# Optimization experiments

Measured on AMD Instinct MI355X. Metric: run time of the kernel, lower is better.

Reference implementation:

```python
import jax, jax.numpy as jnp
import numpy as np

H = 4  # head_num
K_CONV = 1  # convolution_num


def mhsa_mean(x, Wq, Wk, Wv, Wo):
    # x: [..., L, d]; standard multi-head self-attention followed by mean over L
    d = x.shape[-1]
    hd = d // H
    q = (x @ Wq).reshape(x.shape[:-1] + (H, hd))
    k = (x @ Wk).reshape(x.shape[:-1] + (H, hd))
    v = (x @ Wv).reshape(x.shape[:-1] + (H, hd))
    scores = jnp.einsum('...lhd,...mhd->...hlm', q, k) / jnp.sqrt(jnp.asarray(hd, x.dtype))
    attn = jax.nn.softmax(scores, axis=-1)
    o = jnp.einsum('...hlm,...mhd->...lhd', attn, v).reshape(x.shape) @ Wo
    return o.mean(axis=-2)


def setup_inputs() -> dict:
    key = jax.random.key(0)
    ks = jax.random.split(key, 18)
    WORD, QUERY, ENT, REV = 50000, 50000, 100000, 100000
    DW, DE = 64, 64
    LQ, LR, E, B = 8, 8, 2000000, 1024
    W_word = jax.random.normal(ks[0], (WORD, DW), jnp.float32) * 0.02
    W_word = W_word.at[0].set(0.0)  # padding_idx=0
    W_query = jax.random.normal(ks[1], (QUERY, DE), jnp.float32) * 0.02
    W_entity = jax.random.normal(ks[2], (ENT, DE), jnp.float32) * 0.02
    Wq = jax.random.normal(ks[3], (DW, DW), jnp.float32) * 0.05
    Wk = jax.random.normal(ks[4], (DW, DW), jnp.float32) * 0.05
    Wv = jax.random.normal(ks[5], (DW, DW), jnp.float32) * 0.05
    Wo = jax.random.normal(ks[6], (DW, DW), jnp.float32) * 0.05
    query_word_ids = jax.random.randint(ks[7], (QUERY, LQ), 0, WORD)
    review_word_ids = jax.random.randint(ks[8], (REV, LR), 0, WORD)
    profile_dst = jax.random.randint(ks[9], (REV,), 0, ENT)
    p_src = jax.random.randint(ks[10], (E,), 0, ENT)
    p_dst = jax.random.randint(ks[11], (E,), 0, ENT)
    p_qid = jax.random.randint(ks[12], (E,), 0, QUERY)
    users = jax.random.randint(ks[13], (B,), 0, ENT)
    items = jax.random.randint(ks[14], (B,), 0, ENT)
    negs = jax.random.randint(ks[15], (B,), 0, ENT)
    query_words = jax.random.randint(ks[16], (B, LQ), 0, WORD)
    return {'W_word': W_word, 'W_query': W_query, 'W_entity': W_entity,
            'Wq': Wq, 'Wk': Wk, 'Wv': Wv, 'Wo': Wo,
            'query_word_ids': query_word_ids, 'review_word_ids': review_word_ids,
            'profile_dst': profile_dst, 'p_src': p_src, 'p_dst': p_dst, 'p_qid': p_qid,
            'users': users, 'items': items, 'negs': negs, 'query_words': query_words}


def reference(W_word, W_query, W_entity, Wq, Wk, Wv, Wo,
              query_word_ids, review_word_ids, profile_dst, p_src, p_dst, p_qid,
              users, items, negs, query_words):
    N = W_entity.shape[0]
    DE = W_query.shape[1]
    # --- doc embeddings via MHSA+mean over composing words ---
    h_query = mhsa_mean(W_word[query_word_ids], Wq, Wk, Wv, Wo)    # [Q, DW]
    h_review = mhsa_mean(W_word[review_word_ids], Wq, Wk, Wv, Wo)  # [R, DW]
    # --- profiles: sum reviews into entities, degree-normalize ---
    deg_p = jnp.maximum(jax.ops.segment_sum(jnp.ones(profile_dst.shape[0], jnp.float32), profile_dst, num_segments=N), 1.0)
    ent_h = jax.ops.segment_sum(h_review, profile_dst, num_segments=N) / deg_p[:, None]
    q_e0 = jnp.concatenate([W_query, h_query], axis=-1)   # [Q, D]
    e_k = jnp.concatenate([W_entity, ent_h], axis=-1)     # e_0 [N, D]
    # --- interaction degrees: out-deg(purchased) + out-deg(purchased_by) ---
    ones_e = jnp.ones(p_src.shape[0], jnp.float32)
    deg_i = jax.ops.segment_sum(ones_e, p_src, num_segments=N) + jax.ops.segment_sum(ones_e, p_dst, num_segments=N)
    inv_sqrt = 1.0 / jnp.sqrt(jnp.maximum(deg_i, 1.0))    # [N]
    q_edge = q_e0[p_qid]                                   # [E, D]
    e_acc = e_k
    for _ in range(K_CONV):
        # purchased: m = src.e_k + q_e0[q_id] / sqrt(deg_i[src]); sum to dst
        msg = e_k[p_src] + q_edge * inv_sqrt[p_src][:, None]
        agg = jax.ops.segment_sum(msg, p_dst, num_segments=N)
        # purchased_by (reverse edges): m = e_k[src]/sqrt(deg_i[src]); sum to dst
        agg = agg + jax.ops.segment_sum(e_k[p_dst] * inv_sqrt[p_dst][:, None], p_src, num_segments=N)
        e_k = agg * inv_sqrt[:, None]
        e_acc = e_acc + e_k
    e = e_acc / (K_CONV + 1)                               # [N, D]
    # --- batch forward (train mode) ---
    qb = mhsa_mean(W_word[query_words], Wq, Wk, Wv, Wo)    # [B, DW]
    qb = jnp.concatenate([jnp.zeros((qb.shape[0], DE), qb.dtype), qb], axis=-1)
    personalized = e[users] + qb
    return personalized, e[items], e[negs]
```

## Files before the change

kernel.cpp:

```cpp
#include <hip/hip_runtime.h>

typedef unsigned int uint;
typedef unsigned short ushort;

typedef __bf16 bf16x8 __attribute__((ext_vector_type(8)));
typedef float f32x4 __attribute__((ext_vector_type(4)));
union U8 { uint4 u4; uint w[4]; bf16x8 b; };

__device__ __forceinline__ float bf2f(ushort u) {
    return __uint_as_float(((uint)u) << 16);
}
__device__ __forceinline__ float2 bfp2f(uint u) {
    float2 r;
    r.x = __uint_as_float(u << 16);
    r.y = __uint_as_float(u & 0xffff0000u);
    return r;
}
__device__ __forceinline__ ushort f2bf(float f) {
    uint u = __float_as_uint(f);
    return (ushort)((u + 0x7fffu + ((u >> 16) & 1u)) >> 16);
}
__device__ __forceinline__ uint4 pack8(float4 a, float4 b) {
    uint4 u;
    u.x = (uint)f2bf(a.x) | ((uint)f2bf(a.y) << 16);
    u.y = (uint)f2bf(a.z) | ((uint)f2bf(a.w) << 16);
    u.z = (uint)f2bf(b.x) | ((uint)f2bf(b.y) << 16);
    u.w = (uint)f2bf(b.z) | ((uint)f2bf(b.w) << 16);
    return u;
}

__global__ void setup_kernel(const float* __restrict__ Wq,
                             const float* __restrict__ Wk,
                             const float* __restrict__ Wv,
                             const float* __restrict__ Wo,
                             ushort* __restrict__ wsw, ushort* __restrict__ wswo,
                             const int* __restrict__ users,
                             const int* __restrict__ items,
                             const int* __restrict__ negs,
                             int* __restrict__ mapid, int* __restrict__ mcnt,
                             int B) {
    int bid = blockIdx.x;
    if (bid < 64) {
        int e = bid * 256 + threadIdx.x;
        if (e < 12288) {
            int f = e >> 9, r = e & 511;
            int lane = r >> 3, i = r & 7;
            int ct = f >> 1, kh = f & 1;
            int k = kh * 32 + (lane >> 4) * 8 + i;
            int col = (ct & 3) * 16 + (lane & 15);
            const float* W = ct < 4 ? Wq : (ct < 8 ? Wk : Wv);
            wsw[f * 512 + lane * 8 + i] = f2bf(W[k * 64 + col]);
        } else if (e < 16384) {
            int e2 = e - 12288;
            int f = e2 >> 9, r = e2 & 511;
            int lane = r >> 3, i = r & 7;
            int ct = f >> 1, kh = f & 1;
            int k = kh * 32 + (lane >> 4) * 8 + i;
            int col = ct * 16 + (lane & 15);
            wswo[f * 512 + lane * 8 + i] = f2bf(Wo[k * 64 + col]);
        }
        return;
    }
    int t = (bid - 64) * 256 + threadIdx.x;
    if (t >= 3 * B) return;
    int n = t < B ? users[t] : (t < 2 * B ? items[t - B] : negs[t - 2 * B]);
    int old = atomicCAS(&mapid[n], -1, -2);
    if (old == -1) mapid[n] = atomicAdd(mcnt, 1);
}

__global__ void pre_kernel(const float* __restrict__ W_word,
                           const ushort* __restrict__ wsw,
                           ushort* __restrict__ Pq, ushort* __restrict__ Pk,
                           ushort* __restrict__ Pv,
                           const float* __restrict__ W_query,
                           const float* __restrict__ W_entity,
                           ushort* __restrict__ qe0b, ushort* __restrict__ e0b,
                           const int* __restrict__ p_src,
                           const int* __restrict__ p_dst,
                           const int* __restrict__ profile_dst,
                           const int* __restrict__ mapid,
                           int* __restrict__ degp, int* __restrict__ deg2,
                           int WORD, int Qn, int N, int E, int R,
                           int nc_blk, int npj_blk, int ncq_blk, int nce_blk) {
    int bid = blockIdx.x;
    int g = bid >> 3, j = bid & 7;
    if ((g & 3) == 3) {
        int idx = (g >> 2) * 8 + j;
        if (idx >= nc_blk) return;
        int base = idx * 1024 + threadIdx.x;
#pragma unroll
        for (int k = 0; k < 4; k++) {
            int t = base + k * 256;
            if (t < E) {
                int s = p_src[t], d = p_dst[t];
                int md = mapid[d]; if (md >= 0) atomicAdd(&deg2[md], 1);
                int ms = mapid[s]; if (ms >= 0) atomicAdd(&deg2[ms], 1);
            }
            if (t < R) atomicAdd(&degp[profile_dst[t]], 1);
        }
        return;
    }
    int idx = ((g >> 2) * 3 + (g & 3)) * 8 + j;
    if (idx < npj_blk) {
        int tile = idx * 4 + (threadIdx.x >> 6);
        if (tile * 16 >= WORD) return;
        int lane = threadIdx.x & 63, l15 = lane & 15, gi = lane >> 4;
        const float* xr = W_word + ((size_t)tile * 16 + l15) * 64 + gi * 8;
        U8 a0, a1;
        a0.u4 = pack8(*(const float4*)(xr), *(const float4*)(xr + 4));
        a1.u4 = pack8(*(const float4*)(xr + 32), *(const float4*)(xr + 36));
        const f32x4 zero4 = {0.f, 0.f, 0.f, 0.f};
#pragma unroll
        for (int ct = 0; ct < 12; ct++) {
            U8 b0, b1;
            b0.u4 = *(const uint4*)(wsw + (ct * 2 + 0) * 512 + lane * 8);
            b1.u4 = *(const uint4*)(wsw + (ct * 2 + 1) * 512 + lane * 8);
            f32x4 acc = __builtin_amdgcn_mfma_f32_16x16x32_bf16(a0.b, b0.b, zero4, 0, 0, 0);
            acc = __builtin_amdgcn_mfma_f32_16x16x32_bf16(a1.b, b1.b, acc, 0, 0, 0);
            ushort* dst = ct < 4 ? Pq : (ct < 8 ? Pk : Pv);
            int col = (ct & 3) * 16 + l15;
#pragma unroll
            for (int r = 0; r < 4; r++)
                dst[((size_t)tile * 16 + gi * 4 + r) * 64 + col] = f2bf(acc[r]);
        }
    } else if (idx < npj_blk + ncq_blk) {
        int t = (idx - npj_blk) * 256 + threadIdx.x;
        if (t >= Qn * 16) return;
        int r = t >> 4, c = (t & 15) * 4;
        const float4 v = *(const float4*)(W_query + (size_t)r * 64 + c);
        ushort4 o;
        o.x = f2bf(v.x); o.y = f2bf(v.y); o.z = f2bf(v.z); o.w = f2bf(v.w);
        *(ushort4*)(qe0b + (size_t)r * 128 + c) = o;
    } else if (idx < npj_blk + ncq_blk + nce_blk) {
        int t = (idx - npj_blk - ncq_blk) * 256 + threadIdx.x;
        if (t >= N * 16) return;
        int r = t >> 4, c = (t & 15) * 4;
        const float4 v = *(const float4*)(W_entity + (size_t)r * 64 + c);
        ushort4 o;
        o.x = f2bf(v.x); o.y = f2bf(v.y); o.z = f2bf(v.z); o.w = f2bf(v.w);
        *(ushort4*)(e0b + (size_t)r * 128 + c) = o;
    }
}

__global__ void scan_sum(const int* __restrict__ degp, int* __restrict__ csum,
                         int N) {
    __shared__ int red[4];
    int chunk = blockIdx.x, t = threadIdx.x;
    int base = chunk * 1024;
    int v = 0;
#pragma unroll
    for (int k = 0; k < 4; k++) {
        int idx = base + t * 4 + k;
        if (idx < N) v += degp[idx];
    }
#pragma unroll
    for (int o = 32; o; o >>= 1) v += __shfl_down(v, o, 64);
    if ((t & 63) == 0) red[t >> 6] = v;
    __syncthreads();
    if (t == 0) csum[chunk] = red[0] + red[1] + red[2] + red[3];
}

__global__ void scan_mid(int* __restrict__ csum, int nchunk,
                         const int* __restrict__ deg2,
                         int* __restrict__ offs2, int* __restrict__ cursor2,
                         int nb2) {
    __shared__ int lds[256];
    int t = threadIdx.x;
    int v = (t < nchunk) ? csum[t] : 0;
    lds[t] = v;
    __syncthreads();
    for (int o = 1; o < 256; o <<= 1) {
        int u = (t >= o) ? lds[t - o] : 0;
        __syncthreads();
        lds[t] += u;
        __syncthreads();
    }
    if (t < nchunk) csum[t] = lds[t] - v;
    __syncthreads();
    int k2 = nb2 >> 8;
    int s = 0;
    for (int k = 0; k < k2; k++) s += deg2[t * k2 + k];
    lds[t] = s;
    __syncthreads();
    for (int o = 1; o < 256; o <<= 1) {
        int u = (t >= o) ? lds[t - o] : 0;
        __syncthreads();
        lds[t] += u;
        __syncthreads();
    }
    int tb = lds[t] - s;
    for (int k = 0; k < k2; k++) {
        int dv = deg2[t * k2 + k];
        offs2[t * k2 + k] = tb;
        cursor2[t * k2 + k] = tb;
        tb += dv;
    }
    if (t == 255) offs2[nb2] = tb;
}

__global__ void scan_chunk(const int* __restrict__ degp,
                           const int* __restrict__ csum,
                           int* __restrict__ offs_r, int* __restrict__ cursor_r,
                           int N) {
    __shared__ int lds[256];
    int chunk = blockIdx.x, t = threadIdx.x;
    int base = chunk * 1024 + t * 4;
    int v0 = (base + 0 < N) ? degp[base + 0] : 0;
    int v1 = (base + 1 < N) ? degp[base + 1] : 0;
    int v2 = (base + 2 < N) ? degp[base + 2] : 0;
    int v3 = (base + 3 < N) ? degp[base + 3] : 0;
    int s = v0 + v1 + v2 + v3;
    lds[t] = s;
    __syncthreads();
    for (int o = 1; o < 256; o <<= 1) {
        int u = (t >= o) ? lds[t - o] : 0;
        __syncthreads();
        lds[t] += u;
        __syncthreads();
    }
    int tb = lds[t] - s + csum[chunk];
    int vv[4] = {v0, v1, v2, v3};
#pragma unroll
    for (int k = 0; k < 4; k++) {
        int idx = base + k;
        if (idx < N) {
            offs_r[idx] = tb; cursor_r[idx] = tb; tb += vv[k];
            if (idx == N - 1) offs_r[N] = tb;
        }
    }
}

__device__ __forceinline__ void mhsa_pair(const ushort* __restrict__ Pq,
                                          const ushort* __restrict__ Pk,
                                          const ushort* __restrict__ Pv,
                                          const int* __restrict__ ids,
                                          int wid2, int lane,
                                          ushort* __restrict__ outb) {
    const int l15 = lane & 15;
    const int gi  = lane >> 4;
    const int hs  = gi >> 1;
    const int dbase = (gi & 1) * 8;
    const int* idr = ids + (size_t)wid2 * 16;
    const bool valid = hs == (l15 >> 3);

    const int myid = idr[l15];
    int vid[8];
#pragma unroll
    for (int i = 0; i < 8; i++) vid[i] = idr[dbase + i];

    uint pk4[4][2];
    const f32x4 zero4 = {0.f, 0.f, 0.f, 0.f};
#pragma unroll
    for (int h = 0; h < 4; h++) {
        U8 a, b;
        if (valid) {
            a.u4 = *(const uint4*)(Pk + (size_t)myid * 64 + h * 16 + dbase);
            b.u4 = *(const uint4*)(Pq + (size_t)myid * 64 + h * 16 + dbase);
        } else {
            a.u4 = make_uint4(0, 0, 0, 0);
            b.u4 = make_uint4(0, 0, 0, 0);
        }
        f32x4 d = __builtin_amdgcn_mfma_f32_16x16x32_bf16(a.b, b.b, zero4, 0, 0, 0);
        float s0 = d[0] * 0.25f, s1 = d[1] * 0.25f;
        float s2 = d[2] * 0.25f, s3 = d[3] * 0.25f;
        if (!valid) { s0 = s1 = s2 = s3 = -1e30f; }
        float mx = fmaxf(fmaxf(s0, s1), fmaxf(s2, s3));
        mx = fmaxf(mx, __shfl_xor(mx, 16, 64));
        mx = fmaxf(mx, __shfl_xor(mx, 32, 64));
        float x0 = __expf(s0 - mx), x1 = __expf(s1 - mx);
        float x2 = __expf(s2 - mx), x3 = __expf(s3 - mx);
        float sm = x0 + x1 + x2 + x3;
        sm += __shfl_xor(sm, 16, 64);
        sm += __shfl_xor(sm, 32, 64);
        float f = 0.125f / sm;
        uint w0 = (uint)f2bf(x0 * f) | ((uint)f2bf(x1 * f) << 16);
        uint w1 = (uint)f2bf(x2 * f) | ((uint)f2bf(x3 * f) << 16);
        pk4[h][0] = valid ? w0 : 0u;
        pk4[h][1] = valid ? w1 : 0u;
    }

    const int srcA = l15 + (gi & 1) * 32;
    const int srcB = srcA + 16;
    const bool hi = gi >= 2;
    size_t vb[8];
#pragma unroll
    for (int i = 0; i < 8; i++) vb[i] = (size_t)vid[i] * 64;
#pragma unroll
    for (int t = 0; t < 4; t++) {
        uint aw0 = (uint)__shfl((int)pk4[t][0], srcA, 64);
        uint aw1 = (uint)__shfl((int)pk4[t][1], srcA, 64);
        uint aw2 = (uint)__shfl((int)pk4[t][0], srcB, 64);
        uint aw3 = (uint)__shfl((int)pk4[t][1], srcB, 64);
        U8 av_;
        av_.w[0] = hi ? 0u : aw0; av_.w[1] = hi ? 0u : aw1;
        av_.w[2] = hi ? 0u : aw2; av_.w[3] = hi ? 0u : aw3;
        uint e[8];
#pragma unroll
        for (int i = 0; i < 8; i++)
            e[i] = hi ? 0u : (uint)Pv[vb[i] + t * 16 + l15];
        U8 bv;
        bv.w[0] = e[0] | (e[1] << 16);
        bv.w[1] = e[2] | (e[3] << 16);
        bv.w[2] = e[4] | (e[5] << 16);
        bv.w[3] = e[6] | (e[7] << 16);
        f32x4 acc = __builtin_amdgcn_mfma_f32_16x16x32_bf16(av_.b, bv.b, zero4, 0, 0, 0);
        float s = acc[0] + acc[1] + acc[2] + acc[3];
        s += __shfl_xor(s, 16, 64);
        if ((gi & 1) == 0) {
            int row = wid2 * 2 + hs;
            outb[(size_t)row * 64 + t * 16 + l15] = f2bf(s);
        }
    }
}

__global__ void mega_kernel(const ushort* __restrict__ Pq,
                            const ushort* __restrict__ Pk,
                            const ushort* __restrict__ Pv,
                            const int* __restrict__ query_word_ids,
                            const int* __restrict__ review_word_ids,
                            const int* __restrict__ query_words,
                            ushort* __restrict__ hqom,
                            ushort* __restrict__ hrev,
                            ushort* __restrict__ omb,
                            const int* __restrict__ p_src,
                            const int* __restrict__ p_dst,
                            const int* __restrict__ p_qid,
                            const int* __restrict__ profile_dst,
                            const int* __restrict__ mapid,
                            int* __restrict__ degc8,
                            int* __restrict__ cursor2, int2* __restrict__ list2,
                            int* __restrict__ cursor_r, int* __restrict__ rmsg,
                            int Qn, int R, int B, int E, int N,
                            int nr_blk, int nq_blk, int nb_blk,
                            int nd_blk, int np_blk, int nv_blk) {
    int bid = blockIdx.x;
    int g = bid >> 3, j = bid & 7;
    int idx = (g >> 1) * 8 + j;
    if (g & 1) {
        if (idx < nd_blk) {
            int* degc = degc8 + (size_t)(bid & 7) * N;
            int base = idx * 1024 + threadIdx.x;
#pragma unroll
            for (int k = 0; k < 4; k++) {
                int t = base + k * 256;
                if (t < E) {
                    atomicAdd(&degc[p_src[t]], 1);
                    atomicAdd(&degc[p_dst[t]], 1);
                }
            }
        } else if (idx < nd_blk + np_blk) {
            int base = (idx - nd_blk) * 512 + threadIdx.x;
#pragma unroll
            for (int k = 0; k < 2; k++) {
                int e = base + k * 256;
                if (e < E) {
                    int s = p_src[e], d = p_dst[e];
                    int md = mapid[d], ms = mapid[s];
                    if (md >= 0)
                        list2[atomicAdd(&cursor2[md], 1)] = make_int2(s, p_qid[e]);
                    if (ms >= 0)
                        list2[atomicAdd(&cursor2[ms], 1)] = make_int2(d, -1);
                }
            }
        } else if (idx < nd_blk + np_blk + nv_blk) {
            int r = (idx - nd_blk - np_blk) * 256 + threadIdx.x;
            if (r >= R) return;
            rmsg[atomicAdd(&cursor_r[profile_dst[r]], 1)] = r;
        }
        return;
    }
    int lane = threadIdx.x & 63;
    int w = threadIdx.x >> 6;
    if (idx < nr_blk) {
        int wid2 = idx * 4 + w;
        if (wid2 < (R >> 1))
            mhsa_pair(Pq, Pk, Pv, review_word_ids, wid2, lane, hrev);
    } else if (idx < nr_blk + nq_blk) {
        int wid2 = (idx - nr_blk) * 4 + w;
        if (wid2 < (Qn >> 1))
            mhsa_pair(Pq, Pk, Pv, query_word_ids, wid2, lane, hqom);
    } else if (idx < nr_blk + nq_blk + nb_blk) {
        int wid2 = (idx - nr_blk - nq_blk) * 4 + w;
        if (wid2 < (B >> 1))
            mhsa_pair(Pq, Pk, Pv, query_words, wid2, lane, omb);
    }
}

__device__ __forceinline__ void wo_tile(int tile,
                                        const ushort* __restrict__ eom,
                                        const ushort* __restrict__ hqom,
                                        const ushort* __restrict__ omb,
                                        const ushort* __restrict__ wswo,
                                        ushort* __restrict__ e0b,
                                        ushort* __restrict__ qe0b,
                                        float* __restrict__ qb,
                                        int N, int Qn, int lane) {
    int l15 = lane & 15, gi = lane >> 4;
    int row0 = tile << 4;
    int region; int rb;
    const ushort* src;
    if (row0 < N)            { region = 0; rb = row0;            src = eom; }
    else if (row0 < N + Qn)  { region = 1; rb = row0 - N;        src = hqom; }
    else                     { region = 2; rb = row0 - N - Qn;   src = omb; }
    const ushort* sr = src + ((size_t)rb + l15) * 64;
    U8 a0, a1;
    a0.u4 = *(const uint4*)(sr + gi * 8);
    a1.u4 = *(const uint4*)(sr + 32 + gi * 8);
    const f32x4 zero4 = {0.f, 0.f, 0.f, 0.f};
#pragma unroll
    for (int ct = 0; ct < 4; ct++) {
        U8 b0, b1;
        b0.u4 = *(const uint4*)(wswo + (ct * 2 + 0) * 512 + lane * 8);
        b1.u4 = *(const uint4*)(wswo + (ct * 2 + 1) * 512 + lane * 8);
        f32x4 acc = __builtin_amdgcn_mfma_f32_16x16x32_bf16(a0.b, b0.b, zero4, 0, 0, 0);
        acc = __builtin_amdgcn_mfma_f32_16x16x32_bf16(a1.b, b1.b, acc, 0, 0, 0);
        int col = ct * 16 + l15;
#pragma unroll
        for (int r = 0; r < 4; r++) {
            int row = rb + gi * 4 + r;
            if (region == 0)      e0b[(size_t)row * 128 + 64 + col] = f2bf(acc[r]);
            else if (region == 1) qe0b[(size_t)row * 128 + 64 + col] = f2bf(acc[r]);
            else                  qb[(size_t)row * 64 + col] = acc[r];
        }
    }
}

__global__ void post1_kernel(const ushort* __restrict__ hrev,
                             const int* __restrict__ offs_r,
                             const int* __restrict__ rmsg,
                             ushort* __restrict__ eom,
                             const ushort* __restrict__ hqom,
                             const ushort* __restrict__ omb,
                             const ushort* __restrict__ wswo,
                             ushort* __restrict__ e0b, ushort* __restrict__ qe0b,
                             float* __restrict__ qb,
                             const int* __restrict__ degc8,
                             float* __restrict__ inv,
                             int N, int Qn, int B,
                             int nent_blk, int nwo_blk) {
    int bid = blockIdx.x;
    if (bid < nent_blk) {
        int g = (bid * 256 + (int)threadIdx.x) >> 4;
        int c = (threadIdx.x & 15) * 4;
        if (g >= N) return;
        int beg = offs_r[g], end = offs_r[g + 1];
        float a0 = 0.f, a1 = 0.f, a2 = 0.f, a3 = 0.f;
        for (int m = beg; m < end; m++) {
            int r = rmsg[m];
            ushort4 v = *(const ushort4*)(hrev + (size_t)r * 64 + c);
            a0 += bf2f(v.x); a1 += bf2f(v.y); a2 += bf2f(v.z); a3 += bf2f(v.w);
        }
        float s = 1.0f / (float)max(end - beg, 1);
        ushort4 o;
        o.x = f2bf(a0 * s); o.y = f2bf(a1 * s); o.z = f2bf(a2 * s); o.w = f2bf(a3 * s);
        *(ushort4*)(eom + (size_t)g * 64 + c) = o;
    } else if (bid < nent_blk + nwo_blk) {
        int ntile = (N + Qn + B) >> 4;
        int tile = (N >> 4) + (bid - nent_blk) * 4 + ((int)threadIdx.x >> 6);
        if (tile >= ntile) return;
        wo_tile(tile, eom, hqom, omb, wswo, e0b, qe0b, qb, N, Qn,
                threadIdx.x & 63);
    } else {
        int t = (bid - nent_blk - nwo_blk) * 256 + threadIdx.x;
        if (t >= N) return;
        int s = 0;
#pragma unroll
        for (int c = 0; c < 8; c++) s += degc8[(size_t)c * N + t];
        inv[t] = 1.0f / sqrtf((float)max(s, 1));
    }
}

__global__ void post2_kernel(const ushort* __restrict__ eom,
                             const ushort* __restrict__ hqom,
                             const ushort* __restrict__ omb,
                             const ushort* __restrict__ wswo,
                             ushort* __restrict__ e0b, ushort* __restrict__ qe0b,
                             float* __restrict__ qb, int N, int Qn, int B) {
    int tile = blockIdx.x * 4 + ((int)threadIdx.x >> 6);
    if (tile >= (N >> 4)) return;
    wo_tile(tile, eom, hqom, omb, wswo, e0b, qe0b, qb, N, Qn, threadIdx.x & 63);
}

__global__ void gather_out(const ushort* __restrict__ e0b,
                           const ushort* __restrict__ qe0b,
                           const float* __restrict__ inv,
                           const int* __restrict__ mapid,
                           const int* __restrict__ offs2,
                           const int2* __restrict__ list2,
                           const float* __restrict__ qb,
                           const int* __restrict__ users,
                           const int* __restrict__ items,
                           const int* __restrict__ negs,
                           float* __restrict__ out, int B) {
    int slot = (blockIdx.x * blockDim.x + threadIdx.x) >> 4;
    int c = (threadIdx.x & 15) * 8;
    if (slot >= 3 * B) return;
    int which = slot / B, b = slot - which * B;
    int node = which == 0 ? users[b] : (which == 1 ? items[b] : negs[b]);
    int m = mapid[node];
    int beg = offs2[m], end = offs2[m + 1];
    float a0 = 0.f, a1 = 0.f, a2 = 0.f, a3 = 0.f;
    float a4 = 0.f, a5 = 0.f, a6 = 0.f, a7 = 0.f;
    for (int i = beg; i < end; i++) {
        int2 mm = list2[i];
        float w = inv[mm.x];
        const uint4 ev = *(const uint4*)(e0b + (size_t)mm.x * 128 + c);
        if (mm.y >= 0) {
            const uint4 qv = *(const uint4*)(qe0b + (size_t)mm.y * 128 + c);
            float2 e, q;
            e = bfp2f(ev.x); q = bfp2f(qv.x); a0 += fmaf(q.x, w, e.x); a1 += fmaf(q.y, w, e.y);
            e = bfp2f(ev.y); q = bfp2f(qv.y); a2 += fmaf(q.x, w, e.x); a3 += fmaf(q.y, w, e.y);
            e = bfp2f(ev.z); q = bfp2f(qv.z); a4 += fmaf(q.x, w, e.x); a5 += fmaf(q.y, w, e.y);
            e = bfp2f(ev.w); q = bfp2f(qv.w); a6 += fmaf(q.x, w, e.x); a7 += fmaf(q.y, w, e.y);
        } else {
            float2 e;
            e = bfp2f(ev.x); a0 = fmaf(e.x, w, a0); a1 = fmaf(e.y, w, a1);
            e = bfp2f(ev.y); a2 = fmaf(e.x, w, a2); a3 = fmaf(e.y, w, a3);
            e = bfp2f(ev.z); a4 = fmaf(e.x, w, a4); a5 = fmaf(e.y, w, a5);
            e = bfp2f(ev.w); a6 = fmaf(e.x, w, a6); a7 = fmaf(e.y, w, a7);
        }
    }
    float wn = inv[node];
    const uint4 sv = *(const uint4*)(e0b + (size_t)node * 128 + c);
    float2 e0v;
    float r0, r1, r2, r3, r4, r5, r6, r7;
    e0v = bfp2f(sv.x); r0 = 0.5f * fmaf(a0, wn, e0v.x); r1 = 0.5f * fmaf(a1, wn, e0v.y);
    e0v = bfp2f(sv.y); r2 = 0.5f * fmaf(a2, wn, e0v.x); r3 = 0.5f * fmaf(a3, wn, e0v.y);
    e0v = bfp2f(sv.z); r4 = 0.5f * fmaf(a4, wn, e0v.x); r5 = 0.5f * fmaf(a5, wn, e0v.y);
    e0v = bfp2f(sv.w); r6 = 0.5f * fmaf(a6, wn, e0v.x); r7 = 0.5f * fmaf(a7, wn, e0v.y);
    if (which == 0 && c >= 64) {
        const float4 q0 = *(const float4*)(qb + (size_t)b * 64 + (c - 64));
        const float4 q1 = *(const float4*)(qb + (size_t)b * 64 + (c - 60));
        r0 += q0.x; r1 += q0.y; r2 += q0.z; r3 += q0.w;
        r4 += q1.x; r5 += q1.y; r6 += q1.z; r7 += q1.w;
    }
    float* dst = out + (size_t)which * B * 128 + (size_t)b * 128 + c;
    float4 w0; w0.x = r0; w0.y = r1; w0.z = r2; w0.w = r3;
    float4 w1; w1.x = r4; w1.y = r5; w1.z = r6; w1.w = r7;
    *(float4*)dst = w0;
    *(float4*)(dst + 4) = w1;
}

extern "C" void kernel_launch(void* const* d_in, const int* in_sizes, int n_in,
                              void* d_out, int out_size, void* d_ws, size_t ws_size,
                              hipStream_t stream) {
    const float* W_word   = (const float*)d_in[0];
    const float* W_query  = (const float*)d_in[1];
    const float* W_entity = (const float*)d_in[2];
    const float* Wq       = (const float*)d_in[3];
    const float* Wk       = (const float*)d_in[4];
    const float* Wv       = (const float*)d_in[5];
    const float* Wo       = (const float*)d_in[6];
    const int* query_word_ids  = (const int*)d_in[7];
    const int* review_word_ids = (const int*)d_in[8];
    const int* profile_dst     = (const int*)d_in[9];
    const int* p_src  = (const int*)d_in[10];
    const int* p_dst  = (const int*)d_in[11];
    const int* p_qid  = (const int*)d_in[12];
    const int* users  = (const int*)d_in[13];
    const int* items  = (const int*)d_in[14];
    const int* negs   = (const int*)d_in[15];
    const int* query_words = (const int*)d_in[16];

    const int WORD = in_sizes[0] / 64;
    const int Qn   = in_sizes[1] / 64;
    const int N    = in_sizes[2] / 64;
    const int R    = in_sizes[8] / 8;
    const int E    = in_sizes[10];
    const int B    = in_sizes[13];

    const int NB2 = ((3 * B + 255) / 256) * 256;

    ushort* e0b  = (ushort*)d_ws;
    ushort* qe0b = e0b + (size_t)N * 128;
    ushort* Pq   = qe0b + (size_t)Qn * 128;
    ushort* Pk   = Pq + (size_t)WORD * 64;
    ushort* Pv   = Pk + (size_t)WORD * 64;
    ushort* hrev = Pv + (size_t)WORD * 64;
    ushort* hqom = hrev + (size_t)R * 64;
    ushort* omb  = hqom + (size_t)Qn * 64;
    ushort* eom  = omb + (size_t)B * 64;
    ushort* wsw  = eom + (size_t)N * 64;
    ushort* wswo = wsw + 12288;
    float*  qb   = (float*)(wswo + 4096);
    float*  inv  = qb + (size_t)B * 64;
    int* degc8    = (int*)(inv + N);
    int* degp     = degc8 + 8 * (size_t)N;
    int* deg2     = degp + N;
    int* mcnt     = deg2 + NB2;
    int* mapid    = mcnt + 4;
    int* offs_r   = mapid + N;
    int* cursor_r = offs_r + N + 2;
    int* csum     = cursor_r + N;
    int* offs2    = csum + 256;
    int* cursor2  = offs2 + NB2 + 2;
    int* rmsg     = cursor2 + NB2;
    int2* list2   = (int2*)(rmsg + R);

    const int nchunk = (N + 1023) / 1024;

    hipMemsetAsync(degc8, 0, (9 * (size_t)N + NB2 + 4) * sizeof(int), stream);
    hipMemsetAsync(mapid, 0xFF, (size_t)N * sizeof(int), stream);

    setup_kernel<<<64 + (3 * B + 255) / 256, 256, 0, stream>>>(
        Wq, Wk, Wv, Wo, wsw, wswo, users, items, negs, mapid, mcnt, B);

    {
        int nc_blk  = (E + 1023) / 1024;
        int npj_blk = (WORD / 16 + 3) / 4;
        int ncq_blk = (Qn * 16 + 255) / 256;
        int nce_blk = (N * 16 + 255) / 256;
        int mh_fam  = npj_blk + ncq_blk + nce_blk;
        int T = max(4 * nc_blk, (mh_fam * 4 + 2) / 3);
        T = ((T + 31) / 32) * 32;
        pre_kernel<<<T, 256, 0, stream>>>(W_word, wsw, Pq, Pk, Pv,
                                          W_query, W_entity, qe0b, e0b,
                                          p_src, p_dst, profile_dst, mapid,
                                          degp, deg2,
                                          WORD, Qn, N, E, R,
                                          nc_blk, npj_blk, ncq_blk, nce_blk);
    }

    scan_sum<<<nchunk, 256, 0, stream>>>(degp, csum, N);
    scan_mid<<<1, 256, 0, stream>>>(csum, nchunk, deg2, offs2, cursor2, NB2);
    scan_chunk<<<nchunk, 256, 0, stream>>>(degp, csum, offs_r, cursor_r, N);

    {
        int nr_blk = (R / 2 + 3) / 4;
        int nq_blk = (Qn / 2 + 3) / 4;
        int nb_blk = (B / 2 + 3) / 4;
        int nd_blk = (E + 1023) / 1024;
        int np_blk = (E + 511) / 512;
        int nv_blk = (R + 255) / 256;
        int sc = nd_blk + np_blk + nv_blk;
        int mh = nr_blk + nq_blk + nb_blk;
        int T = 2 * max(sc, mh);
        T = ((T + 31) / 32) * 32;
        mega_kernel<<<T, 256, 0, stream>>>(Pq, Pk, Pv,
                                           query_word_ids, review_word_ids, query_words,
                                           hqom, hrev, omb,
                                           p_src, p_dst, p_qid, profile_dst, mapid,
                                           degc8, cursor2, list2, cursor_r, rmsg,
                                           Qn, R, B, E, N,
                                           nr_blk, nq_blk, nb_blk,
                                           nd_blk, np_blk, nv_blk);
    }

    {
        int nent_blk = (N * 16 + 255) / 256;
        int ntile12 = (Qn + B) / 16 + 1;
        int nwo_blk = (ntile12 + 3) / 4;
        int ninv_blk = (N + 255) / 256;
        post1_kernel<<<nent_blk + nwo_blk + ninv_blk, 256, 0, stream>>>(
            hrev, offs_r, rmsg, eom, hqom, omb, wswo, e0b, qe0b, qb,
            degc8, inv, N, Qn, B, nent_blk, nwo_blk);
    }

    post2_kernel<<<(N / 16 + 3) / 4, 256, 0, stream>>>(eom, hqom, omb, wswo,
                                                       e0b, qe0b, qb, N, Qn, B);

    gather_out<<<(3 * B * 16 + 255) / 256, 256, 0, stream>>>(e0b, qe0b, inv,
                                                             mapid, offs2, list2,
                                                             qb, users, items, negs,
                                                             (float*)d_out, B);
}
```

Measured before the change: 488.3 us.

## Filter edges with shared-memory node bitmap and split degree counting across kernels

Builds a global bitmap of batch nodes (users/items/negs) during setup. Each edge-scanning block copies it into LDS and tests membership there, so most edges skip the random mapid lookup. Full-degree counting moves from eight replicated counters summed later to a single counter array, with half the edges counted in pre_kernel and half in mega_kernel. The list-building blocks each process more edges, and the launch grids are rebalanced. The cost is a 12.5KB LDS bitmap load per block and more atomic contention on the single degree array.

Result: faster. 411.0 us (-15.8%).

```diff
diff --git a/kernel.cpp b/kernel.cpp
--- a/kernel.cpp
+++ b/kernel.cpp
@@ -28,6 +28,8 @@
     u.w = (uint)f2bf(b.z) | ((uint)f2bf(b.w) << 16);
     return u;
 }
+
+#define NBM 3136
 
 __global__ void setup_kernel(const float* __restrict__ Wq,
                              const float* __restrict__ Wk,
@@ -38,7 +40,7 @@
                              const int* __restrict__ items,
                              const int* __restrict__ negs,
                              int* __restrict__ mapid, int* __restrict__ mcnt,
-                             int B) {
+                             uint* __restrict__ gbm, int B) {
     int bid = blockIdx.x;
     if (bid < 64) {
         int e = bid * 256 + threadIdx.x;
@@ -64,6 +66,7 @@
     int t = (bid - 64) * 256 + threadIdx.x;
     if (t >= 3 * B) return;
     int n = t < B ? users[t] : (t < 2 * B ? items[t - B] : negs[t - 2 * B]);
+    atomicOr(&gbm[n >> 5], 1u << (n & 31));
     int old = atomicCAS(&mapid[n], -1, -2);
     if (old == -1) mapid[n] = atomicAdd(mcnt, 1);
 }
@@ -79,22 +82,32 @@
                            const int* __restrict__ p_dst,
                            const int* __restrict__ profile_dst,
                            const int* __restrict__ mapid,
+                           const uint* __restrict__ gbm,
+                           int* __restrict__ degc,
                            int* __restrict__ degp, int* __restrict__ deg2,
-                           int WORD, int Qn, int N, int E, int R,
+                           int WORD, int Qn, int N, int E, int Ehalf, int R,
                            int nc_blk, int npj_blk, int ncq_blk, int nce_blk) {
+    __shared__ uint bm[NBM];
     int bid = blockIdx.x;
     int g = bid >> 3, j = bid & 7;
     if ((g & 3) == 3) {
         int idx = (g >> 2) * 8 + j;
         if (idx >= nc_blk) return;
+        int nbm = (N + 31) >> 5;
+        for (int i = threadIdx.x; i < nbm; i += 256) bm[i] = gbm[i];
+        __syncthreads();
         int base = idx * 1024 + threadIdx.x;
 #pragma unroll
         for (int k = 0; k < 4; k++) {
             int t = base + k * 256;
             if (t < E) {
                 int s = p_src[t], d = p_dst[t];
-                int md = mapid[d]; if (md >= 0) atomicAdd(&deg2[md], 1);
-                int ms = mapid[s]; if (ms >= 0) atomicAdd(&deg2[ms], 1);
+                if (t < Ehalf) {
+                    atomicAdd(&degc[s], 1);
+                    atomicAdd(&degc[d], 1);
+                }
+                if ((bm[d >> 5] >> (d & 31)) & 1u) atomicAdd(&deg2[mapid[d]], 1);
+                if ((bm[s >> 5] >> (s & 31)) & 1u) atomicAdd(&deg2[mapid[s]], 1);
             }
             if (t < R) atomicAdd(&degp[profile_dst[t]], 1);
         }
@@ -327,19 +340,20 @@
                             const int* __restrict__ p_qid,
                             const int* __restrict__ profile_dst,
                             const int* __restrict__ mapid,
-                            int* __restrict__ degc8,
+                            const uint* __restrict__ gbm,
+                            int* __restrict__ degc,
                             int* __restrict__ cursor2, int2* __restrict__ list2,
                             int* __restrict__ cursor_r, int* __restrict__ rmsg,
-                            int Qn, int R, int B, int E, int N,
+                            int Qn, int R, int B, int E, int Ehalf, int N,
                             int nr_blk, int nq_blk, int nb_blk,
-                            int nd_blk, int np_blk, int nv_blk) {
+                            int ndh_blk, int npl_blk, int nv_blk) {
+    __shared__ uint bm[NBM];
     int bid = blockIdx.x;
     int g = bid >> 3, j = bid & 7;
-    int idx = (g >> 1) * 8 + j;
-    if (g & 1) {
-        if (idx < nd_blk) {
-            int* degc = degc8 + (size_t)(bid & 7) * N;
-            int base = idx * 1024 + threadIdx.x;
+    if ((g & 3) == 3) {
+        int idx = (g >> 2) * 8 + j;
+        if (idx < ndh_blk) {
+            int base = Ehalf + idx * 1024 + threadIdx.x;
 #pragma unroll
             for (int k = 0; k < 4; k++) {
                 int t = base + k * 256;
@@ -348,27 +362,34 @@
                     atomicAdd(&degc[p_dst[t]], 1);
                 }
             }
-        } else if (idx < nd_blk + np_blk) {
-            int base = (idx - nd_blk) * 512 + threadIdx.x;
-#pragma unroll
-            for (int k = 0; k < 2; k++) {
+        } else if (idx < ndh_blk + npl_blk) {
+            int nbm = (N + 31) >> 5;
+            for (int i = threadIdx.x; i < nbm; i += 256) bm[i] = gbm[i];
+            __syncthreads();
+            int base = (idx - ndh_blk) * 2048 + threadIdx.x;
+#pragma unroll
+            for (int k = 0; k < 8; k++) {
                 int e = base + k * 256;
                 if (e < E) {
                     int s = p_src[e], d = p_dst[e];
-                    int md = mapid[d], ms = mapid[s];
-                    if (md >= 0)
+                    if ((bm[d >> 5] >> (d & 31)) & 1u) {
+                        int md = mapid[d];
                         list2[atomicAdd(&cursor2[md], 1)] = make_int2(s, p_qid[e]);
-                    if (ms >= 0)
+                    }
+                    if ((bm[s >> 5] >> (s & 31)) & 1u) {
+                        int ms = mapid[s];
                         list2[atomicAdd(&cursor2[ms], 1)] = make_int2(d, -1);
+                    }
                 }
             }
-        } else if (idx < nd_blk + np_blk + nv_blk) {
-            int r = (idx - nd_blk - np_blk) * 256 + threadIdx.x;
+        } else if (idx < ndh_blk + npl_blk + nv_blk) {
+            int r = (idx - ndh_blk - npl_blk) * 256 + threadIdx.x;
             if (r >= R) return;
             rmsg[atomicAdd(&cursor_r[profile_dst[r]], 1)] = r;
         }
         return;
     }
+    int idx = ((g >> 2) * 3 + (g & 3)) * 8 + j;
     int lane = threadIdx.x & 63;
     int w = threadIdx.x >> 6;
     if (idx < nr_blk) {
@@ -434,7 +455,7 @@
                              const ushort* __restrict__ wswo,
                              ushort* __restrict__ e0b, ushort* __restrict__ qe0b,
                              float* __restrict__ qb,
-                             const int* __restrict__ degc8,
+                             const int* __restrict__ degc,
                              float* __restrict__ inv,
                              int N, int Qn, int B,
                              int nent_blk, int nwo_blk) {
@@ -463,10 +484,7 @@
     } else {
         int t = (bid - nent_blk - nwo_blk) * 256 + threadIdx.x;
         if (t >= N) return;
-        int s = 0;
-#pragma unroll
-        for (int c = 0; c < 8; c++) s += degc8[(size_t)c * N + t];
-        inv[t] = 1.0f / sqrtf((float)max(s, 1));
+        inv[t] = 1.0f / sqrtf((float)max(degc[t], 1));
     }
 }
 
@@ -568,6 +586,7 @@
     const int R    = in_sizes[8] / 8;
     const int E    = in_sizes[10];
     const int B    = in_sizes[13];
+    const int Ehalf = E / 2;
 
     const int NB2 = ((3 * B + 255) / 256) * 256;
 
@@ -584,11 +603,12 @@
     ushort* wswo = wsw + 12288;
     float*  qb   = (float*)(wswo + 4096);
     float*  inv  = qb + (size_t)B * 64;
-    int* degc8    = (int*)(inv + N);
-    int* degp     = degc8 + 8 * (size_t)N;
+    int* degc     = (int*)(inv + N);
+    int* degp     = degc + N;
     int* deg2     = degp + N;
     int* mcnt     = deg2 + NB2;
-    int* mapid    = mcnt + 4;
+    uint* gbm     = (uint*)(mcnt + 4);
+    int* mapid    = (int*)(gbm + 3200);
     int* offs_r   = mapid + N;
     int* cursor_r = offs_r + N + 2;
     int* csum     = cursor_r + N;
@@ -599,11 +619,11 @@
 
     const int nchunk = (N + 1023) / 1024;
 
-    hipMemsetAsync(degc8, 0, (9 * (size_t)N + NB2 + 4) * sizeof(int), stream);
+    hipMemsetAsync(degc, 0, (2 * (size_t)N + NB2 + 4 + 3200) * sizeof(int), stream);
     hipMemsetAsync(mapid, 0xFF, (size_t)N * sizeof(int), stream);
 
     setup_kernel<<<64 + (3 * B + 255) / 256, 256, 0, stream>>>(
-        Wq, Wk, Wv, Wo, wsw, wswo, users, items, negs, mapid, mcnt, B);
+        Wq, Wk, Wv, Wo, wsw, wswo, users, items, negs, mapid, mcnt, gbm, B);
 
     {
         int nc_blk  = (E + 1023) / 1024;
@@ -615,9 +635,9 @@
         T = ((T + 31) / 32) * 32;
         pre_kernel<<<T, 256, 0, stream>>>(W_word, wsw, Pq, Pk, Pv,
                                           W_query, W_entity, qe0b, e0b,
-                                          p_src, p_dst, profile_dst, mapid,
-                                          degp, deg2,
-                                          WORD, Qn, N, E, R,
+                                          p_src, p_dst, profile_dst, mapid, gbm,
+                                          degc, degp, deg2,
+                                          WORD, Qn, N, E, Ehalf, R,
                                           nc_blk, npj_blk, ncq_blk, nce_blk);
     }
 
@@ -629,21 +649,21 @@
         int nr_blk = (R / 2 + 3) / 4;
         int nq_blk = (Qn / 2 + 3) / 4;
         int nb_blk = (B / 2 + 3) / 4;
-        int nd_blk = (E + 1023) / 1024;
-        int np_blk = (E + 511) / 512;
+        int ndh_blk = (E - Ehalf + 1023) / 1024;
+        int npl_blk = (E + 2047) / 2048;
         int nv_blk = (R + 255) / 256;
-        int sc = nd_blk + np_blk + nv_blk;
+        int sc = ndh_blk + npl_blk + nv_blk;
         int mh = nr_blk + nq_blk + nb_blk;
-        int T = 2 * max(sc, mh);
+        int T = max(4 * sc, (mh * 4 + 2) / 3);
         T = ((T + 31) / 32) * 32;
         mega_kernel<<<T, 256, 0, stream>>>(Pq, Pk, Pv,
                                            query_word_ids, review_word_ids, query_words,
                                            hqom, hrev, omb,
                                            p_src, p_dst, p_qid, profile_dst, mapid,
-                                           degc8, cursor2, list2, cursor_r, rmsg,
-                                           Qn, R, B, E, N,
+                                           gbm, degc, cursor2, list2, cursor_r, rmsg,
+                                           Qn, R, B, E, Ehalf, N,
                                            nr_blk, nq_blk, nb_blk,
-                                           nd_blk, np_blk, nv_blk);
+                                           ndh_blk, npl_blk, nv_blk);
     }
 
     {
@@ -653,7 +673,7 @@
         int ninv_blk = (N + 255) / 256;
         post1_kernel<<<nent_blk + nwo_blk + ninv_blk, 256, 0, stream>>>(
             hrev, offs_r, rmsg, eom, hqom, omb, wswo, e0b, qe0b, qb,
-            degc8, inv, N, Qn, B, nent_blk, nwo_blk);
+            degc, inv, N, Qn, B, nent_blk, nwo_blk);
     }
 
     post2_kernel<<<(N / 16 + 3) / 4, 256, 0, stream>>>(eom, hqom, omb, wswo,
```
